# Kernel tuning notes

Measured on AMD Instinct MI355X. Metric: run time of the kernel, lower is better.

## Reference

```python
import jax, jax.numpy as jnp
import numpy as np

N_LAYERS = 4
B, L, D = 2, 2048, 512
H, E = 8, 64          # n_heads = d_model // d_head
DFF = 1024
EPS = 1e-6
MAX_LOG_SCALE = float(np.log(100.0))   # QKNorm max_scale clamp
LOG10 = float(np.log(10.0))            # QKNorm scale init


def rms_norm(x, scale, eps=EPS):
    # matches torch rms_norm: x * (scale * rsqrt(mean(x^2, -1) + eps))
    ms = jnp.mean(jnp.square(x), axis=-1, keepdims=True)
    return x * (scale * jax.lax.rsqrt(ms + eps))


def rope(x):
    # standard rotary embedding over head dim, half-split convention. x: [n,h,l,e]
    e, l = x.shape[-1], x.shape[-2]
    inv = 1.0 / (10000.0 ** (jnp.arange(0, e, 2, dtype=jnp.float32) / e))
    freqs = jnp.arange(l, dtype=jnp.float32)[:, None] * inv[None, :]   # [l, e/2]
    cos, sin = jnp.cos(freqs), jnp.sin(freqs)
    x1, x2 = x[..., : e // 2], x[..., e // 2:]
    return jnp.concatenate([x1 * cos - x2 * sin, x1 * sin + x2 * cos], axis=-1)


def setup_inputs() -> dict:
    key = jax.random.key(0)
    ks = jax.random.split(key, 10)
    s = 0.02
    return {
        "x": jax.random.normal(ks[0], (B, L, D), jnp.float32),
        "cond": jax.random.normal(ks[1], (B, D), jnp.float32),
        "attn_mask": jnp.ones((B, L), jnp.int32),
        # per-layer stacked params (torch Linear(in,out,bias=False) stored as [in,out], y = x @ W)
        "wn_attn": s * jax.random.normal(ks[2], (N_LAYERS, D, D), jnp.float32),      # AdaRMSNorm cond proj (attn)
        "wqkv": s * jax.random.normal(ks[3], (N_LAYERS, D, 3 * D), jnp.float32),
        "qk_scale": jnp.full((N_LAYERS, H), LOG10, jnp.float32),                     # QKNorm per-head log-scale
        "wout": s * jax.random.normal(ks[4], (N_LAYERS, D, D), jnp.float32),
        "wn_ff": s * jax.random.normal(ks[5], (N_LAYERS, D, D), jnp.float32),        # AdaRMSNorm cond proj (ff)
        "wup": s * jax.random.normal(ks[6], (N_LAYERS, D, 2 * DFF), jnp.float32),
        "wdown": s * jax.random.normal(ks[7], (N_LAYERS, DFF, D), jnp.float32),
        "out_scale": jnp.ones((D,), jnp.float32),                                    # final RMSNorm scale
    }


def forward(x, cond, attn_mask, wn_attn, wqkv, qk_scale, wout, wn_ff, wup, wdown, out_scale):
    n, l, d = x.shape
    # mask bias: (attn_mask != 1) * -1e9, repeated 'n l -> n h l s' (query-dim mask, as in source)
    bias = (attn_mask != 1).astype(x.dtype) * -1e9
    bias = bias[:, None, :, None]  # [n,1,l,1] broadcast over heads and key dim

    def block(h_x, p):
        wn_a, w_qkv, qs, w_o, wn_f, w_up, w_dn = p
        # --- self attention ---
        skip = h_x
        y = rms_norm(h_x, (cond @ wn_a + 1.0)[:, None, :])            # AdaRMSNorm
        qkv = y @ w_qkv                                               # [n,l,3d]
        q, k, v = jnp.split(qkv, 3, axis=-1)
        to_heads = lambda t: t.reshape(n, l, H, E).transpose(0, 2, 1, 3)
        q, k, v = to_heads(q), to_heads(k), to_heads(v)
        qs_c = jnp.minimum(qs, MAX_LOG_SCALE)
        hs = jnp.exp(0.5 * qs_c - 0.25 * np.log(E))[:, None, None]    # [H,1,1] QKNorm scale
        q = rope(rms_norm(q, hs))
        k = rope(rms_norm(k, hs))
        scores = jnp.einsum('nhle,nhse->nhls', q, k) / np.sqrt(E) + bias
        attn = jax.nn.softmax(scores, axis=-1)
        o = jnp.einsum('nhls,nhse->nhle', attn, v)
        o = o.transpose(0, 2, 1, 3).reshape(n, l, d)
        h_x = skip + o @ w_o
        # --- GEGLU feed-forward ---
        skip = h_x
        y = rms_norm(h_x, (cond @ wn_f + 1.0)[:, None, :])
        u = y @ w_up
        a, b = jnp.split(u, 2, axis=-1)
        y = a * jax.nn.gelu(b, approximate=False)                     # F.gelu exact
        h_x = skip + y @ w_dn
        return h_x, None

    x, _ = jax.lax.scan(block, x, (wn_attn, wqkv, qk_scale, wout, wn_ff, wup, wdown))
    return rms_norm(x, out_scale)


def reference(x, cond, attn_mask, wn_attn, wqkv, qk_scale, wout, wn_ff, wup, wdown, out_scale):
    return forward(x, cond, attn_mask, wn_attn, wqkv, qk_scale, wout, wn_ff, wup, wdown, out_scale)
```

## Files before the change

### kernel.cpp

```cpp
#include <hip/hip_runtime.h>
#include <hip/hip_bf16.h>

#define NB 2
#define LL 2048
#define DD 512
#define HH 8
#define EE 64
#define DFF 1024
#define NL 4
#define EPS_F 1e-6f

typedef __bf16 bf16x8 __attribute__((ext_vector_type(8)));
typedef __bf16 bf16x4 __attribute__((ext_vector_type(4)));
typedef float f32x4 __attribute__((ext_vector_type(4)));

__device__ __forceinline__ unsigned short f2bf(float f) {
    unsigned int u = __float_as_uint(f);
    unsigned int r = (u + 0x7FFFu + ((u >> 16) & 1u)) >> 16;
    return (unsigned short)r;
}
__device__ __forceinline__ unsigned short f2bf_t(float f) {
    return (unsigned short)(__float_as_uint(f) >> 16);
}
__device__ __forceinline__ void gload16(const void* g, void* l) {
    __builtin_amdgcn_global_load_lds(
        (const __attribute__((address_space(1))) unsigned int*)g,
        (__attribute__((address_space(3))) unsigned int*)l, 16, 0, 0);
}

__global__ void rope_table_kernel(float* __restrict__ cosT, float* __restrict__ sinT) {
    int idx = blockIdx.x * 256 + threadIdx.x;
    if (idx >= LL * 32) return;
    int l = idx >> 5, i = idx & 31;
    float inv = powf(10000.f, -(float)i * (1.f / 32.f));
    float ang = (float)l * inv;
    cosT[idx] = cosf(ang);
    sinT[idx] = sinf(ang);
}

__global__ __launch_bounds__(256) void wcast_all_kernel(const float* __restrict__ wqkv,
                                                        const float* __restrict__ wout,
                                                        const float* __restrict__ wup,
                                                        const float* __restrict__ wdown,
                                                        unsigned short* __restrict__ wt) {
    int bid = blockIdx.x;
    int layer = bid / 2560, rem = bid % 2560;
    const float* W; unsigned short* WT; int K, N, t;
    if (rem < 768)       { W = wqkv  + (size_t)layer * 786432;  WT = wt + (size_t)layer * 786432;            K = 512;  N = 1536; t = rem; }
    else if (rem < 1024) { W = wout  + (size_t)layer * 262144;  WT = wt + 3145728 + (size_t)layer * 262144;  K = 512;  N = 512;  t = rem - 768; }
    else if (rem < 2048) { W = wup   + (size_t)layer * 1048576; WT = wt + 4194304 + (size_t)layer * 1048576; K = 512;  N = 2048; t = rem - 1024; }
    else                 { W = wdown + (size_t)layer * 524288;  WT = wt + 8388608 + (size_t)layer * 524288;  K = 1024; N = 512;  t = rem - 2048; }
    int tn = N / 32;
    int n0 = (t % tn) * 32, k0 = (t / tn) * 32;
    __shared__ float tile[32][33];
    int r = threadIdx.x >> 5, c = threadIdx.x & 31;
#pragma unroll
    for (int i = 0; i < 4; ++i)
        tile[r + 8 * i][c] = W[(size_t)(k0 + r + 8 * i) * N + n0 + c];
    __syncthreads();
#pragma unroll
    for (int i = 0; i < 4; ++i)
        WT[(size_t)(n0 + r + 8 * i) * K + k0 + c] = f2bf(tile[c][r + 8 * i]);
}

__global__ __launch_bounds__(256) void cond_all_kernel(const float* __restrict__ cond,
                                                       const float* __restrict__ wn_attn,
                                                       const float* __restrict__ wn_ff,
                                                       float* __restrict__ s_all) {
    int bid = blockIdx.x;
    int d0 = (bid & 7) * 64;
    int b = (bid >> 3) & 1;
    int which = (bid >> 4) & 1;
    int layer = bid >> 5;
    const float* W = (which ? wn_ff : wn_attn) + (size_t)layer * DD * DD;
    int t = threadIdx.x;
    int d = d0 + (t & 63), kq = t >> 6;
    const float* c = cond + b * DD + kq * 128;
    const float* Wp = W + (size_t)(kq * 128) * DD + d;
    float s = 0.f;
#pragma unroll 8
    for (int j = 0; j < 128; ++j) s = fmaf(c[j], Wp[(size_t)j * DD], s);
    __shared__ float red[4][64];
    red[kq][t & 63] = s;
    __syncthreads();
    if (t < 64) {
        float tot = 1.f + red[0][t] + red[1][t] + red[2][t] + red[3][t];
        s_all[((size_t)(layer * 2 + which) * NB + b) * DD + d0 + t] = tot;
    }
}

__global__ __launch_bounds__(256) void rmsnorm_bf16_kernel(const float* __restrict__ x,
                                                           const float* __restrict__ scale,
                                                           unsigned short* __restrict__ y) {
    int row = blockIdx.x;
    int b = row >> 11;
    int t = threadIdx.x;
    float2 v = ((const float2*)(x + (size_t)row * DD))[t];
    float ss = v.x * v.x + v.y * v.y;
#pragma unroll
    for (int o = 32; o > 0; o >>= 1) ss += __shfl_xor(ss, o);
    __shared__ float red[4];
    if ((t & 63) == 0) red[t >> 6] = ss;
    __syncthreads();
    float tot = red[0] + red[1] + red[2] + red[3];
    float inv = rsqrtf(tot * (1.f / DD) + EPS_F);
    float2 s2 = ((const float2*)(scale + b * DD))[t];
    unsigned int lo = f2bf(v.x * s2.x * inv);
    unsigned int hi = f2bf(v.y * s2.y * inv);
    ((unsigned int*)(y + (size_t)row * DD))[t] = lo | (hi << 16);
}

__global__ __launch_bounds__(256) void rmsnorm_f32_kernel(const float* __restrict__ x,
                                                          const float* __restrict__ scale,
                                                          float* __restrict__ y) {
    int row = blockIdx.x;
    int t = threadIdx.x;
    float2 v = ((const float2*)(x + (size_t)row * DD))[t];
    float ss = v.x * v.x + v.y * v.y;
#pragma unroll
    for (int o = 32; o > 0; o >>= 1) ss += __shfl_xor(ss, o);
    __shared__ float red[4];
    if ((t & 63) == 0) red[t >> 6] = ss;
    __syncthreads();
    float tot = red[0] + red[1] + red[2] + red[3];
    float inv = rsqrtf(tot * (1.f / DD) + EPS_F);
    float2 s2 = ((const float2*)scale)[t];
    float2 o2;
    o2.x = v.x * s2.x * inv;
    o2.y = v.y * s2.y * inv;
    ((float2*)(y + (size_t)row * DD))[t] = o2;
}

template <int BN>
__global__ __launch_bounds__(256) void gemm_bf16_kernel(const unsigned short* __restrict__ A,
                                                        const unsigned short* __restrict__ BT,
                                                        const float* __restrict__ R,
                                                        float* __restrict__ C,
                                                        int M, int N, int K) {
    constexpr int NJ = BN / 32;
    __shared__ __align__(16) unsigned short As[128 * 32];
    __shared__ __align__(16) unsigned short Bs[BN * 32];
    int tid = threadIdx.x;
    int n0 = blockIdx.x * BN, m0 = blockIdx.y * 128;
    int w = tid >> 6, l = tid & 63;
    int wr = w >> 1, wc = w & 1;
    int kf = 8 * (l >> 4);
    int rf = l & 15;

    f32x4 acc[4][NJ] = {};

    for (int k0 = 0; k0 < K; k0 += 32) {
#pragma unroll
        for (int u = 0; u < 2; ++u) {
            int c = u * 256 + tid;
            int row = c >> 2, ch = c & 3;
            gload16(A + (size_t)(m0 + row) * K + k0 + ch * 8, &As[c * 8]);
        }
#pragma unroll
        for (int u = 0; u < BN / 64; ++u) {
            int c = u * 256 + tid;
            int row = c >> 2, ch = c & 3;
            gload16(BT + (size_t)(n0 + row) * K + k0 + ch * 8, &Bs[c * 8]);
        }
        __syncthreads();

        bf16x8 a[4], b[NJ];
#pragma unroll
        for (int i = 0; i < 4; ++i)
            a[i] = *(const bf16x8*)(&As[(wr * 64 + i * 16 + rf) * 32 + kf]);
#pragma unroll
        for (int j = 0; j < NJ; ++j)
            b[j] = *(const bf16x8*)(&Bs[(wc * (BN / 2) + j * 16 + rf) * 32 + kf]);
#pragma unroll
        for (int i = 0; i < 4; ++i)
#pragma unroll
            for (int j = 0; j < NJ; ++j)
                acc[i][j] = __builtin_amdgcn_mfma_f32_16x16x32_bf16(a[i], b[j], acc[i][j], 0, 0, 0);
        __syncthreads();
    }

    int rl = l >> 4, cl = l & 15;
#pragma unroll
    for (int i = 0; i < 4; ++i)
#pragma unroll
        for (int j = 0; j < NJ; ++j)
#pragma unroll
            for (int r = 0; r < 4; ++r) {
                int row = m0 + wr * 64 + i * 16 + rl * 4 + r;
                int col = n0 + wc * (BN / 2) + j * 16 + cl;
                size_t off = (size_t)row * N + col;
                float v = acc[i][j][r];
                if (R) v += R[off];
                C[off] = v;
            }
}

__global__ __launch_bounds__(256) void gemm_geglu_kernel(const unsigned short* __restrict__ A,
                                                         const unsigned short* __restrict__ BT,
                                                         unsigned short* __restrict__ G) {
    __shared__ __align__(16) unsigned short As[128 * 32];
    __shared__ __align__(16) unsigned short Bs[128 * 32];
    __shared__ float ep[128][65];
    int tid = threadIdx.x;
    int n0 = blockIdx.x * 64, m0 = blockIdx.y * 128;
    int w = tid >> 6, l = tid & 63;
    int wr = w >> 1, wc = w & 1;
    int kf = 8 * (l >> 4);
    int rf = l & 15;

    f32x4 acc[4][4] = {};

    for (int k0 = 0; k0 < DD; k0 += 32) {
#pragma unroll
        for (int u = 0; u < 2; ++u) {
            int c = u * 256 + tid;
            int row = c >> 2, ch = c & 3;
            gload16(A + (size_t)(m0 + row) * DD + k0 + ch * 8, &As[c * 8]);
            int grow = (row < 64) ? (n0 + row) : (DFF + n0 + row - 64);
            gload16(BT + (size_t)grow * DD + k0 + ch * 8, &Bs[c * 8]);
        }
        __syncthreads();

        bf16x8 a[4], b[4];
#pragma unroll
        for (int i = 0; i < 4; ++i)
            a[i] = *(const bf16x8*)(&As[(wr * 64 + i * 16 + rf) * 32 + kf]);
#pragma unroll
        for (int j = 0; j < 4; ++j)
            b[j] = *(const bf16x8*)(&Bs[(wc * 64 + j * 16 + rf) * 32 + kf]);
#pragma unroll
        for (int i = 0; i < 4; ++i)
#pragma unroll
            for (int j = 0; j < 4; ++j)
                acc[i][j] = __builtin_amdgcn_mfma_f32_16x16x32_bf16(a[i], b[j], acc[i][j], 0, 0, 0);
        __syncthreads();
    }

    int rl = l >> 4, cl = l & 15;
    if (wc == 0) {
#pragma unroll
        for (int i = 0; i < 4; ++i)
#pragma unroll
            for (int j = 0; j < 4; ++j)
#pragma unroll
                for (int r = 0; r < 4; ++r)
                    ep[wr * 64 + i * 16 + rl * 4 + r][j * 16 + cl] = acc[i][j][r];
    }
    __syncthreads();
    if (wc == 1) {
#pragma unroll
        for (int i = 0; i < 4; ++i)
#pragma unroll
            for (int j = 0; j < 4; ++j)
#pragma unroll
                for (int r = 0; r < 4; ++r) {
                    int row = wr * 64 + i * 16 + rl * 4 + r;
                    float bv = acc[i][j][r];
                    float av = ep[row][j * 16 + cl];
                    float ge = 0.5f * bv * (1.f + erff(bv * 0.70710678f));
                    G[(size_t)(m0 + row) * DFF + n0 + j * 16 + cl] = f2bf(av * ge);
                }
    }
}

__global__ __launch_bounds__(256) void qkv_prep_kernel(const float* __restrict__ qkv,
                                                       const float* __restrict__ qs,
                                                       const float* __restrict__ cosT,
                                                       const float* __restrict__ sinT,
                                                       unsigned short* __restrict__ qh,
                                                       unsigned short* __restrict__ kh,
                                                       unsigned short* __restrict__ vt) {
    __shared__ float tile[64][65];
    int t = threadIdx.x;
    if (blockIdx.x < 8192) {
        int w = blockIdx.x * 4 + (t >> 6);
        int e = t & 63;
        int h = w & 7;
        int l = (w >> 3) & (LL - 1);
        int b = w >> 14;
        size_t rb = ((size_t)(b * LL + l)) * (3 * DD) + h * EE + e;
        float q = qkv[rb];
        float k = qkv[rb + DD];
        float sq = q * q, sk = k * k;
#pragma unroll
        for (int o = 1; o < 64; o <<= 1) {
            sq += __shfl_xor(sq, o);
            sk += __shfl_xor(sk, o);
        }
        float hsc = expf(0.5f * fminf(qs[h], 4.60517019f) - 1.03972077f) * 0.35355339059f;
        float qn = q * (hsc * 1.44269504f) * rsqrtf(sq * (1.f / EE) + EPS_F);
        float kn = k * hsc * rsqrtf(sk * (1.f / EE) + EPS_F);
        float qp = __shfl_xor(qn, 32);
        float kp = __shfl_xor(kn, 32);
        int i = e & 31;
        float c = cosT[l * 32 + i], s = sinT[l * 32 + i];
        float qo = (e < 32) ? (qn * c - qp * s) : (qp * s + qn * c);
        float ko = (e < 32) ? (kn * c - kp * s) : (kp * s + kn * c);
        size_t ob = ((size_t)((b * HH + h) * LL + l)) * EE + e;
        qh[ob] = f2bf(qo);
        kh[ob] = f2bf(ko);
    } else {
        int bid = blockIdx.x - 8192;
        int lt = bid & 31, bh = bid >> 5;
        int b = bh >> 3, h = bh & 7;
        int l0 = lt * 64;
#pragma unroll
        for (int i = 0; i < 4; ++i) {
            int c = t + i * 256;
            int row = c >> 4, q4 = c & 15;
            float4 v4 = *(const float4*)(qkv + ((size_t)(b * LL + l0 + row)) * (3 * DD) + 2 * DD + h * EE + q4 * 4);
            tile[row][q4 * 4 + 0] = v4.x;
            tile[row][q4 * 4 + 1] = v4.y;
            tile[row][q4 * 4 + 2] = v4.z;
            tile[row][q4 * 4 + 3] = v4.w;
        }
        __syncthreads();
        int e = t >> 2, lc = t & 3;
        unsigned int* dst = (unsigned int*)(vt + ((size_t)(bh * EE + e)) * LL + l0 + lc * 16);
#pragma unroll
        for (int j2 = 0; j2 < 8; ++j2) {
            unsigned int lo = f2bf(tile[lc * 16 + 2 * j2][e]);
            unsigned int hi = f2bf(tile[lc * 16 + 2 * j2 + 1][e]);
            dst[j2] = lo | (hi << 16);
        }
    }
}

#define KVB 32
#define KLDP 68
#define VLDP 44
#define PLDP 36
__global__ __launch_bounds__(256) void flash_mfma_kernel(const unsigned short* __restrict__ qh,
                                                         const unsigned short* __restrict__ kh,
                                                         const unsigned short* __restrict__ vt,
                                                         float* __restrict__ op,
                                                         float* __restrict__ os) {
    __shared__ unsigned short K_lds[32 * KLDP];
    __shared__ unsigned short VT_lds[80 * VLDP];
    __shared__ unsigned short P_lds[4][16 * PLDP];
    int bid = blockIdx.x;
    int qb = bid & 31, h = (bid >> 5) & 7, b = (bid >> 8) & 1, split = bid >> 9;
    int bh = b * HH + h;
    int tid = threadIdx.x, w = tid >> 6, l = tid & 63;
    int lo = l & 15, hi4 = l >> 4;
    int q0 = qb * 64 + w * 16;

    for (int idx = tid; idx < 16 * VLDP; idx += 256) {
        int rr = idx / VLDP;
        VT_lds[(64 + rr) * VLDP + (idx - rr * VLDP)] = (rr == 0) ? 0x3F80 : 0;
    }

    const unsigned short* qbase = qh + ((size_t)bh * LL) * EE;
    bf16x8 qa[2];
#pragma unroll
    for (int s = 0; s < 2; ++s)
        qa[s] = *(const bf16x8*)(qbase + (size_t)(q0 + lo) * EE + s * 32 + 8 * hi4);

    f32x4 oacc[4] = {};
    f32x4 osum = {};

    for (int kt = split * 16; kt < split * 16 + 16; ++kt) {
        int kv0 = kt * KVB;
#pragma unroll
        for (int u = 0; u < 2; ++u) {
            int c = tid + u * 256;
            int arr = c >> 8, cc = c & 255;
            if (arr == 0) {
                int row = cc >> 3, ch = cc & 7;
                *(uint4*)&K_lds[row * KLDP + ch * 8] =
                    *(const uint4*)(kh + ((size_t)bh * LL + kv0 + row) * EE + ch * 8);
            } else {
                int row = cc >> 2, ch = cc & 3;
                *(uint4*)&VT_lds[row * VLDP + ch * 8] =
                    *(const uint4*)(vt + ((size_t)bh * EE + row) * LL + kv0 + ch * 8);
            }
        }
        __syncthreads();

        f32x4 S[2] = {};
        __builtin_amdgcn_s_setprio(1);
#pragma unroll
        for (int nf = 0; nf < 2; ++nf)
#pragma unroll
            for (int s = 0; s < 2; ++s) {
                bf16x8 kb = *(const bf16x8*)&K_lds[(nf * 16 + lo) * KLDP + s * 32 + 8 * hi4];
                S[nf] = __builtin_amdgcn_mfma_f32_16x16x32_bf16(qa[s], kb, S[nf], 0, 0, 0);
            }
        __builtin_amdgcn_s_setprio(0);

#pragma unroll
        for (int r = 0; r < 4; ++r)
#pragma unroll
            for (int nf = 0; nf < 2; ++nf)
                P_lds[w][(hi4 * 4 + r) * PLDP + nf * 16 + lo] = f2bf_t(exp2f(S[nf][r]));

        __builtin_amdgcn_s_setprio(1);
        bf16x4 p0 = *(const bf16x4*)&P_lds[w][lo * PLDP + 8 * hi4];
        bf16x4 p1 = *(const bf16x4*)&P_lds[w][lo * PLDP + 8 * hi4 + 4];
        bf16x8 pa;
#pragma unroll
        for (int j = 0; j < 4; ++j) { pa[j] = p0[j]; pa[4 + j] = p1[j]; }
#pragma unroll
        for (int nf = 0; nf < 4; ++nf) {
            bf16x8 vb = *(const bf16x8*)&VT_lds[(nf * 16 + lo) * VLDP + 8 * hi4];
            oacc[nf] = __builtin_amdgcn_mfma_f32_16x16x32_bf16(pa, vb, oacc[nf], 0, 0, 0);
        }
        bf16x8 vbE = *(const bf16x8*)&VT_lds[(64 + lo) * VLDP + 8 * hi4];
        osum = __builtin_amdgcn_mfma_f32_16x16x32_bf16(pa, vbE, osum, 0, 0, 0);
        __builtin_amdgcn_s_setprio(0);
        __syncthreads();
    }

    float* opp = op + (size_t)split * (NB * LL * DD);
#pragma unroll
    for (int r = 0; r < 4; ++r) {
        int row = q0 + hi4 * 4 + r;
        float* optr = opp + ((size_t)(b * LL + row)) * DD + h * EE;
#pragma unroll
        for (int nf = 0; nf < 4; ++nf)
            optr[nf * 16 + lo] = oacc[nf][r];
        if (lo == 0)
            os[split * (NB * HH * LL) + bh * LL + row] = osum[r];
    }
}

__global__ __launch_bounds__(256) void attn_combine_kernel(const float* __restrict__ op,
                                                           const float* __restrict__ os,
                                                           unsigned short* __restrict__ oh) {
    int idx = (blockIdx.x * 256 + threadIdx.x) * 4;
    int col = idx & 511;
    int h = col >> 6;
    int row = (idx >> 9) & (LL - 1);
    int b = idx >> 20;
    int bh = b * HH + h;
    float s = 0.f;
    float4 a = make_float4(0.f, 0.f, 0.f, 0.f);
#pragma unroll
    for (int sp = 0; sp < 4; ++sp) {
        s += os[sp * (NB * HH * LL) + bh * LL + row];
        float4 t = *(const float4*)(op + (size_t)sp * (NB * LL * DD) + idx);
        a.x += t.x; a.y += t.y; a.z += t.z; a.w += t.w;
    }
    float inv = 1.f / s;
    ushort4 o4;
    o4.x = f2bf(a.x * inv);
    o4.y = f2bf(a.y * inv);
    o4.z = f2bf(a.z * inv);
    o4.w = f2bf(a.w * inv);
    *(ushort4*)(oh + idx) = o4;
}

extern "C" void kernel_launch(void* const* d_in, const int* in_sizes, int n_in,
                              void* d_out, int out_size, void* d_ws, size_t ws_size,
                              hipStream_t stream) {
    const float* x        = (const float*)d_in[0];
    const float* cond     = (const float*)d_in[1];
    const float* wn_attn  = (const float*)d_in[3];
    const float* wqkv     = (const float*)d_in[4];
    const float* qk_scale = (const float*)d_in[5];
    const float* wout     = (const float*)d_in[6];
    const float* wn_ff    = (const float*)d_in[7];
    const float* wup      = (const float*)d_in[8];
    const float* wdown    = (const float*)d_in[9];
    const float* out_scale= (const float*)d_in[10];
    float* out = (float*)d_out;

    const int TOK = NB * LL;
    const size_t nHx = (size_t)TOK * DD;
    const size_t M = 1024 * 1024;

    float* ws = (float*)d_ws;
    float* hx  = ws;
    unsigned short* y_bf = (unsigned short*)(ws + 2 * M);
    float* qkv = ws + 3 * M;
    float* op  = ws + 3 * M;
    unsigned short* qh_bf = (unsigned short*)(ws + 11 * M);
    unsigned short* g_bf  = (unsigned short*)(ws + 11 * M);
    unsigned short* kh_bf = (unsigned short*)(ws + 12 * M);
    unsigned short* vt_bf = (unsigned short*)(ws + 13 * M);
    unsigned short* oh_bf = (unsigned short*)(ws + 14 * M);
    unsigned short* wt = (unsigned short*)(ws + 15 * M);
    float* smal  = ws + 20 * M;
    float* s_all = smal;
    float* os    = smal + 8192;
    float* cosT  = os + 131072;
    float* sinT  = cosT + 65536;

    hipMemcpyAsync(hx, x, nHx * sizeof(float), hipMemcpyDeviceToDevice, stream);
    rope_table_kernel<<<256, 256, 0, stream>>>(cosT, sinT);
    cond_all_kernel<<<128, 256, 0, stream>>>(cond, wn_attn, wn_ff, s_all);
    wcast_all_kernel<<<10240, 256, 0, stream>>>(wqkv, wout, wup, wdown, wt);

    unsigned short* wqkvT  = wt;
    unsigned short* woutT  = wt + 3145728;
    unsigned short* wupT   = wt + 4194304;
    unsigned short* wdownT = wt + 8388608;

    for (int layer = 0; layer < NL; ++layer) {
        const float* qs = qk_scale + layer * HH;

        rmsnorm_bf16_kernel<<<TOK, 256, 0, stream>>>(hx, s_all + (size_t)(layer * 2 + 0) * NB * DD, y_bf);
        gemm_bf16_kernel<64><<<dim3(1536 / 64, TOK / 128), 256, 0, stream>>>(
            y_bf, wqkvT + (size_t)layer * 786432, nullptr, qkv, TOK, 1536, 512);
        qkv_prep_kernel<<<8704, 256, 0, stream>>>(qkv, qs, cosT, sinT, qh_bf, kh_bf, vt_bf);
        flash_mfma_kernel<<<2048, 256, 0, stream>>>(qh_bf, kh_bf, vt_bf, op, os);
        attn_combine_kernel<<<2048, 256, 0, stream>>>(op, os, oh_bf);
        gemm_bf16_kernel<64><<<dim3(512 / 64, TOK / 128), 256, 0, stream>>>(
            oh_bf, woutT + (size_t)layer * 262144, hx, hx, TOK, 512, 512);

        rmsnorm_bf16_kernel<<<TOK, 256, 0, stream>>>(hx, s_all + (size_t)(layer * 2 + 1) * NB * DD, y_bf);
        gemm_geglu_kernel<<<dim3(16, 32), 256, 0, stream>>>(
            y_bf, wupT + (size_t)layer * 1048576, g_bf);
        gemm_bf16_kernel<64><<<dim3(512 / 64, TOK / 128), 256, 0, stream>>>(
            g_bf, wdownT + (size_t)layer * 524288, hx, hx, TOK, 512, 1024);
    }
    rmsnorm_f32_kernel<<<TOK, 256, 0, stream>>>(hx, out_scale, out);
}
```

Before: 655.1 us.

## Double-buffer LDS tiles in GEMM kernels and retune flash attention LDS padding

Both the generic bf16 GEMM and the fused GEGLU GEMM now keep two LDS buffers and issue the global loads for the next K-tile before computing on the current one, so load latency can overlap with MFMA work. The GEGLU kernel aliases the A/B staging buffers with the epilogue scratch array so that double buffering does not raise its LDS footprint. The flash attention kernel's K and V^T LDS row paddings are changed to alter bank-conflict behaviour. The added LDS in the generic GEMM may lower occupancy, and the aliasing depends on the trailing sync in the loop before the epilogue writes.

```diff
diff --git a/kernel.cpp b/kernel.cpp
--- a/kernel.cpp
+++ b/kernel.cpp
@@ -138,8 +138,8 @@
                                                         float* __restrict__ C,
                                                         int M, int N, int K) {
     constexpr int NJ = BN / 32;
-    __shared__ __align__(16) unsigned short As[128 * 32];
-    __shared__ __align__(16) unsigned short Bs[BN * 32];
+    __shared__ __align__(16) unsigned short As[2][128 * 32];
+    __shared__ __align__(16) unsigned short Bs[2][BN * 32];
     int tid = threadIdx.x;
     int n0 = blockIdx.x * BN, m0 = blockIdx.y * 128;
     int w = tid >> 6, l = tid & 63;
@@ -147,30 +147,36 @@
     int kf = 8 * (l >> 4);
     int rf = l & 15;
 
-    f32x4 acc[4][NJ] = {};
-
-    for (int k0 = 0; k0 < K; k0 += 32) {
+    auto stage = [&](int buf, int k0) {
 #pragma unroll
         for (int u = 0; u < 2; ++u) {
             int c = u * 256 + tid;
             int row = c >> 2, ch = c & 3;
-            gload16(A + (size_t)(m0 + row) * K + k0 + ch * 8, &As[c * 8]);
+            gload16(A + (size_t)(m0 + row) * K + k0 + ch * 8, &As[buf][c * 8]);
         }
 #pragma unroll
         for (int u = 0; u < BN / 64; ++u) {
             int c = u * 256 + tid;
             int row = c >> 2, ch = c & 3;
-            gload16(BT + (size_t)(n0 + row) * K + k0 + ch * 8, &Bs[c * 8]);
-        }
-        __syncthreads();
-
+            gload16(BT + (size_t)(n0 + row) * K + k0 + ch * 8, &Bs[buf][c * 8]);
+        }
+    };
+
+    f32x4 acc[4][NJ] = {};
+    const int nt = K / 32;
+    stage(0, 0);
+    __syncthreads();
+
+    for (int t = 0; t < nt; ++t) {
+        if (t + 1 < nt) stage((t + 1) & 1, (t + 1) * 32);
+        int cur = t & 1;
         bf16x8 a[4], b[NJ];
 #pragma unroll
         for (int i = 0; i < 4; ++i)
-            a[i] = *(const bf16x8*)(&As[(wr * 64 + i * 16 + rf) * 32 + kf]);
+            a[i] = *(const bf16x8*)(&As[cur][(wr * 64 + i * 16 + rf) * 32 + kf]);
 #pragma unroll
         for (int j = 0; j < NJ; ++j)
-            b[j] = *(const bf16x8*)(&Bs[(wc * (BN / 2) + j * 16 + rf) * 32 + kf]);
+            b[j] = *(const bf16x8*)(&Bs[cur][(wc * (BN / 2) + j * 16 + rf) * 32 + kf]);
 #pragma unroll
         for (int i = 0; i < 4; ++i)
 #pragma unroll
@@ -198,9 +204,10 @@
 __global__ __launch_bounds__(256) void gemm_geglu_kernel(const unsigned short* __restrict__ A,
                                                          const unsigned short* __restrict__ BT,
                                                          unsigned short* __restrict__ G) {
-    __shared__ __align__(16) unsigned short As[128 * 32];
-    __shared__ __align__(16) unsigned short Bs[128 * 32];
-    __shared__ float ep[128][65];
+    __shared__ __align__(16) unsigned char smem[128 * 65 * sizeof(float)];
+    unsigned short* As = (unsigned short*)smem;
+    unsigned short* Bs = (unsigned short*)(smem + 16384);
+    float* ep = (float*)smem;
     int tid = threadIdx.x;
     int n0 = blockIdx.x * 64, m0 = blockIdx.y * 128;
     int w = tid >> 6, l = tid & 63;
@@ -208,26 +215,31 @@
     int kf = 8 * (l >> 4);
     int rf = l & 15;
 
-    f32x4 acc[4][4] = {};
-
-    for (int k0 = 0; k0 < DD; k0 += 32) {
+    auto stage = [&](int buf, int k0) {
 #pragma unroll
         for (int u = 0; u < 2; ++u) {
             int c = u * 256 + tid;
             int row = c >> 2, ch = c & 3;
-            gload16(A + (size_t)(m0 + row) * DD + k0 + ch * 8, &As[c * 8]);
+            gload16(A + (size_t)(m0 + row) * DD + k0 + ch * 8, &As[buf * 4096 + c * 8]);
             int grow = (row < 64) ? (n0 + row) : (DFF + n0 + row - 64);
-            gload16(BT + (size_t)grow * DD + k0 + ch * 8, &Bs[c * 8]);
-        }
-        __syncthreads();
-
+            gload16(BT + (size_t)grow * DD + k0 + ch * 8, &Bs[buf * 4096 + c * 8]);
+        }
+    };
+
+    f32x4 acc[4][4] = {};
+    stage(0, 0);
+    __syncthreads();
+
+    for (int t = 0; t < 16; ++t) {
+        if (t + 1 < 16) stage((t + 1) & 1, (t + 1) * 32);
+        int cur = t & 1;
         bf16x8 a[4], b[4];
 #pragma unroll
         for (int i = 0; i < 4; ++i)
-            a[i] = *(const bf16x8*)(&As[(wr * 64 + i * 16 + rf) * 32 + kf]);
+            a[i] = *(const bf16x8*)(&As[cur * 4096 + (wr * 64 + i * 16 + rf) * 32 + kf]);
 #pragma unroll
         for (int j = 0; j < 4; ++j)
-            b[j] = *(const bf16x8*)(&Bs[(wc * 64 + j * 16 + rf) * 32 + kf]);
+            b[j] = *(const bf16x8*)(&Bs[cur * 4096 + (wc * 64 + j * 16 + rf) * 32 + kf]);
 #pragma unroll
         for (int i = 0; i < 4; ++i)
 #pragma unroll
@@ -244,7 +256,7 @@
             for (int j = 0; j < 4; ++j)
 #pragma unroll
                 for (int r = 0; r < 4; ++r)
-                    ep[wr * 64 + i * 16 + rl * 4 + r][j * 16 + cl] = acc[i][j][r];
+                    ep[(wr * 64 + i * 16 + rl * 4 + r) * 65 + j * 16 + cl] = acc[i][j][r];
     }
     __syncthreads();
     if (wc == 1) {
@@ -256,7 +268,7 @@
                 for (int r = 0; r < 4; ++r) {
                     int row = wr * 64 + i * 16 + rl * 4 + r;
                     float bv = acc[i][j][r];
-                    float av = ep[row][j * 16 + cl];
+                    float av = ep[row * 65 + j * 16 + cl];
                     float ge = 0.5f * bv * (1.f + erff(bv * 0.70710678f));
                     G[(size_t)(m0 + row) * DFF + n0 + j * 16 + cl] = f2bf(av * ge);
                 }
@@ -327,8 +339,8 @@
 }
 
 #define KVB 32
-#define KLDP 68
-#define VLDP 44
+#define KLDP 72
+#define VLDP 40
 #define PLDP 36
 __global__ __launch_bounds__(256) void flash_mfma_kernel(const unsigned short* __restrict__ qh,
                                                          const unsigned short* __restrict__ kh,
```

Result: faster. 614.3 us (-6.2%).
